# Optimization experiments

Hardware: AMD Instinct MI355X
Metric: run time of the kernel (lower is better)

The kernel has to match this reference:

```python
import jax, jax.numpy as jnp
import numpy as np

SELF_OBS_DIM = 18
NBR_OBS_DIM = 6
K = 6          # num_use_neighbor_obs
H = 128        # neighbor_hidden_size
B = 65536


def _mlp2(x, w1, b1, w2, b2):
    # two fc layers each followed by tanh nonlinearity
    x = jnp.tanh(x @ w1 + b1)
    return jnp.tanh(x @ w2 + b2)


def setup_inputs() -> dict:
    key = jax.random.key(0)
    ks = jax.random.split(key, 12)

    def w(k, i, o):
        return jax.random.normal(k, (i, o), dtype=jnp.float32) * (1.0 / np.sqrt(i))

    return {
        "self_obs": jax.random.normal(ks[0], (B, SELF_OBS_DIM), dtype=jnp.float32),
        "obs": jax.random.normal(ks[1], (B, SELF_OBS_DIM + K * NBR_OBS_DIM), dtype=jnp.float32),
        # embedding_mlp: (self_obs_dim + nbr_obs_dim) -> H -> H
        "e_w1": w(ks[2], SELF_OBS_DIM + NBR_OBS_DIM, H), "e_b1": jnp.zeros((H,), jnp.float32),
        "e_w2": w(ks[3], H, H), "e_b2": jnp.zeros((H,), jnp.float32),
        # neighbor_value_mlp: H -> H -> H
        "v_w1": w(ks[4], H, H), "v_b1": jnp.zeros((H,), jnp.float32),
        "v_w2": w(ks[5], H, H), "v_b2": jnp.zeros((H,), jnp.float32),
        # attention_mlp: 2H -> H -> H -> 1
        "a_w1": w(ks[6], 2 * H, H), "a_b1": jnp.zeros((H,), jnp.float32),
        "a_w2": w(ks[7], H, H), "a_b2": jnp.zeros((H,), jnp.float32),
        "a_w3": w(ks[8], H, 1), "a_b3": jnp.zeros((1,), jnp.float32),
        "all_neighbor_obs_size": K * NBR_OBS_DIM,
        "batch_size": B,
    }


def reference(self_obs, obs, e_w1, e_b1, e_w2, e_b2, v_w1, v_b1, v_w2, v_b2,
              a_w1, a_b1, a_w2, a_b2, a_w3, a_b3, all_neighbor_obs_size, batch_size):
    # slice neighbor obs and flatten: row i -> (batch i//K, neighbor i%K)
    obs_neighbors = obs[:, SELF_OBS_DIM:SELF_OBS_DIM + all_neighbor_obs_size]
    obs_neighbors = obs_neighbors.reshape(-1, NBR_OBS_DIM)            # [B*K, 6]
    # torch .repeat(K, 1): tile whole batch K times -> row i -> batch i % B
    self_obs_repeat = jnp.tile(self_obs, (K, 1))                       # [B*K, 18]
    mlp_input = jnp.concatenate((self_obs_repeat, obs_neighbors), axis=1)

    neighbor_embeddings = _mlp2(mlp_input, e_w1, e_b1, e_w2, e_b2)     # [B*K, H]
    neighbor_values = _mlp2(neighbor_embeddings, v_w1, v_b1, v_w2, v_b2)

    emb_mean = jnp.mean(neighbor_embeddings.reshape(batch_size, -1, H), axis=1)  # [B, H]
    emb_mean_repeat = jnp.tile(emb_mean, (K, 1))                       # [B*K, H]

    att_in = jnp.concatenate((neighbor_embeddings, emb_mean_repeat), axis=1)     # [B*K, 2H]
    att_h = jnp.tanh(att_in @ a_w1 + a_b1)
    att_h = jnp.tanh(att_h @ a_w2 + a_b2)
    att_logits = (att_h @ a_w3 + a_b3).reshape(batch_size, -1)         # [B, K]

    att = jax.nn.softmax(att_logits, axis=1).reshape(-1, 1)            # [B*K, 1]
    weighted = (att * neighbor_values).reshape(batch_size, -1, H)      # [B, K, H]
    return jnp.sum(weighted, axis=1)                                   # [B, H]
```

## Files before the change

kernel.cpp:

```cpp
#include <hip/hip_runtime.h>

typedef _Float16 f16;
typedef f16   f16x8 __attribute__((ext_vector_type(8)));
typedef float f32x4 __attribute__((ext_vector_type(4)));
typedef unsigned int uint;

#define NB     65536
#define NROWS  (NB*6)
#define NTILES 4096
#define TPB    16

#define OFF_E1 0
#define OFF_E2 4096
#define OFF_V1 20480
#define OFF_V2 36864
#define OFF_A1 53248
#define OFF_A2 86016
#define WFRAG_TOTAL 102400

#define EMB_BYTE_OFF   204800ull
#define MEANH_BYTE_OFF (204800ull + 100663296ull)

#define LDS_FENCE() asm volatile("s_waitcnt lgkmcnt(0)" ::: "memory")
#define WAIT_VM0()  asm volatile("s_waitcnt vmcnt(0)" ::: "memory")
#define BAR()       { __builtin_amdgcn_s_barrier(); __builtin_amdgcn_sched_barrier(0); }

__device__ __forceinline__ float tanh_fast(float x) {
  float e = __expf(2.0f * x);
  return 1.0f - 2.0f * __builtin_amdgcn_rcpf(e + 1.0f);
}

__global__ void prep_weights(const float* __restrict__ e1, const float* __restrict__ e2,
                             const float* __restrict__ v1, const float* __restrict__ v2,
                             const float* __restrict__ a1, const float* __restrict__ a2,
                             f16* __restrict__ dst)
{
  int i = blockIdx.x * 256 + threadIdx.x;
  if (i >= WFRAG_TOTAL) return;
  const float* src; int base, Ksrc;
  if      (i < OFF_E2) { src = e1; base = OFF_E1; Ksrc = 24;  }
  else if (i < OFF_V1) { src = e2; base = OFF_E2; Ksrc = 128; }
  else if (i < OFF_V2) { src = v1; base = OFF_V1; Ksrc = 128; }
  else if (i < OFF_A1) { src = v2; base = OFF_V2; Ksrc = 128; }
  else if (i < OFF_A2) { src = a1; base = OFF_A1; Ksrc = 256; }
  else                 { src = a2; base = OFF_A2; Ksrc = 128; }
  int li   = i - base;
  int j    = li & 7;
  int lane = (li >> 3) & 63;
  int nt   = (li >> 9) & 7;
  int kc   = li >> 12;
  int k = kc*32 + (lane >> 4)*8 + j;
  int n = nt*16 + (lane & 15);
  float v = (k < Ksrc) ? src[k*128 + n] : 0.0f;
  dst[i] = (f16)v;
}

__device__ __forceinline__ void mfma2(f32x4* acc, f16x8 a0, f16x8 a1, const f16* Wb, int lane)
{
  #pragma unroll
  for (int nt = 0; nt < 8; ++nt) {
    f16x8 w = *(const f16x8*)(Wb + (nt*64 + lane)*8);
    acc[nt] = __builtin_amdgcn_mfma_f32_16x16x32_f16(a0, w, acc[nt], 0, 0, 0);
  }
  #pragma unroll
  for (int nt = 0; nt < 8; ++nt) {
    f16x8 w = *(const f16x8*)(Wb + ((8+nt)*64 + lane)*8);
    acc[nt] = __builtin_amdgcn_mfma_f32_16x16x32_f16(a1, w, acc[nt], 0, 0, 0);
  }
}

__device__ __forceinline__ void epi_tanh_store(char* tb, const f32x4* acc, const float* bias8,
                                               int wid, int lane)
{
  int col0 = lane & 15, q = lane >> 4;
  #pragma unroll
  for (int nt = 0; nt < 8; ++nt) {
    #pragma unroll
    for (int rg = 0; rg < 4; ++rg) {
      int row = wid*16 + q*4 + rg;
      float h = tanh_fast(acc[nt][rg] + bias8[nt]);
      int byte = (row*256 + (nt*16 + col0)*2) ^ ((row & 7) << 4);
      *(f16*)(tb + byte) = (f16)h;
    }
  }
}

__device__ __forceinline__ void read_h_frags(const char* tb, f16x8* frag, int wid, int lane)
{
  int c = lane >> 4, rr = lane & 15;
  int row = wid*16 + rr;
  #pragma unroll
  for (int kc = 0; kc < 4; ++kc) {
    int byte = (row*256 + kc*64 + c*16) ^ ((row & 7) << 4);
    frag[kc] = *(const f16x8*)(tb + byte);
  }
}

__device__ __forceinline__ void gload_lds16(const f16* g, f16* l) {
  __builtin_amdgcn_global_load_lds(
    (const __attribute__((address_space(1))) unsigned int*)g,
    (__attribute__((address_space(3))) unsigned int*)l, 16, 0, 0);
}

__device__ __forceinline__ f16x8 gather_x(const float* __restrict__ so, const float* __restrict__ obs,
                                          int r, int c)
{
  int rs = r & (NB - 1);
  uint rq = (uint)r / 6u;
  uint rm = (uint)r - rq*6u;
  float xv[8] = {0.f,0.f,0.f,0.f,0.f,0.f,0.f,0.f};
  if (c == 0) {
    #pragma unroll
    for (int j = 0; j < 8; ++j) xv[j] = so[rs*18 + j];
  } else if (c == 1) {
    #pragma unroll
    for (int j = 0; j < 8; ++j) xv[j] = so[rs*18 + 8 + j];
  } else if (c == 2) {
    xv[0] = so[rs*18 + 16];
    xv[1] = so[rs*18 + 17];
    const float* nb = obs + (size_t)rq*54 + 18 + rm*6;
    #pragma unroll
    for (int j = 0; j < 6; ++j) xv[2+j] = nb[j];
  }
  f16x8 f;
  #pragma unroll
  for (int j = 0; j < 8; ++j) f[j] = (f16)xv[j];
  return f;
}

__global__ void __launch_bounds__(384, 1) enc_kernel(
  const float* __restrict__ self_obs, const float* __restrict__ obs,
  const float* __restrict__ e_b1, const float* __restrict__ e_b2,
  const float* __restrict__ a_b1,
  const f16* __restrict__ wfrag, f16* __restrict__ emb_out, f16* __restrict__ meanh_out)
{
  __shared__ __align__(16) f16 wE1[4096];
  __shared__ __align__(16) f16 wE2[16384];
  __shared__ __align__(16) f16 wA1m[16384];
  __shared__ __align__(16) char tbuf[24576];
  __shared__ __align__(16) char mbuf[4096];

  int tid = threadIdx.x, lane = tid & 63, wid = tid >> 6;
  int c = lane >> 4, rr = lane & 15;

  #pragma unroll
  for (int it = 0; it < 2; ++it) { int idx = it*384 + tid; if (idx < 512)  gload_lds16(wfrag + OFF_E1 + idx*8, wE1 + idx*8); }
  #pragma unroll
  for (int it = 0; it < 6; ++it) { int idx = it*384 + tid; if (idx < 2048) gload_lds16(wfrag + OFF_E2 + idx*8, wE2 + idx*8); }
  #pragma unroll
  for (int it = 0; it < 6; ++it) { int idx = it*384 + tid; if (idx < 2048) gload_lds16(wfrag + OFF_A1 + 16384 + idx*8, wA1m + idx*8); }

  float b1r[8], b2r[8], ab1r[8];
  #pragma unroll
  for (int nt = 0; nt < 8; ++nt) {
    int col = nt*16 + rr;
    b1r[nt] = e_b1[col]; b2r[nt] = e_b2[col]; ab1r[nt] = a_b1[col];
  }

  int t0 = blockIdx.x * TPB;
  f16x8 xfrag = gather_x(self_obs, obs, t0*96 + wid*16 + rr, c);
  WAIT_VM0(); BAR();

  for (int i = 0; i < TPB; ++i) {
    int t = t0 + i;
    f32x4 acc[8];
    #pragma unroll
    for (int nt = 0; nt < 8; ++nt) acc[nt] = (f32x4){0.f,0.f,0.f,0.f};
    #pragma unroll
    for (int nt = 0; nt < 8; ++nt) {
      f16x8 w = *(const f16x8*)(wE1 + (nt*64 + lane)*8);
      acc[nt] = __builtin_amdgcn_mfma_f32_16x16x32_f16(xfrag, w, acc[nt], 0, 0, 0);
    }
    epi_tanh_store(tbuf, acc, b1r, wid, lane);
    LDS_FENCE();
    f16x8 hf[4];
    read_h_frags(tbuf, hf, wid, lane);

    f16x8 xnext = gather_x(self_obs, obs,
                           ((i+1 < TPB) ? (t+1) : t0)*96 + wid*16 + rr, c);

    f32x4 acc2[8];
    #pragma unroll
    for (int nt = 0; nt < 8; ++nt) acc2[nt] = (f32x4){0.f,0.f,0.f,0.f};
    mfma2(acc2, hf[0], hf[1], wE2,        lane);
    mfma2(acc2, hf[2], hf[3], wE2 + 8192, lane);
    epi_tanh_store(tbuf, acc2, b2r, wid, lane);
    LDS_FENCE(); BAR();

    size_t gbase = (size_t)t * (96*128);
    #pragma unroll
    for (int it2 = 0; it2 < 4; ++it2) {
      int idx = it2*384 + tid;
      int row = idx >> 4, ch = idx & 15;
      int byte = (row*256 + ch*16) ^ ((row & 7) << 4);
      *(uint4*)(emb_out + gbase + row*128 + ch*8) = *(const uint4*)(tbuf + byte);
    }
    for (int i2 = tid; i2 < 2048; i2 += 384) {
      int b = i2 >> 7, col = i2 & 127;
      float s = 0.f;
      #pragma unroll
      for (int k2 = 0; k2 < 6; ++k2) {
        int brow = b*6 + k2;
        int byte = (brow*256 + col*2) ^ ((brow & 7) << 4);
        s += (float)*(const f16*)(tbuf + byte);
      }
      int mb = (b*256 + col*2) ^ ((b & 7) << 4);
      *(f16*)(mbuf + mb) = (f16)(s * (1.0f/6.0f));
    }
    LDS_FENCE(); BAR();

    f16x8 mfr[4];
    read_h_frags(mbuf, mfr, 0, lane);
    LDS_FENCE(); BAR();
    f32x4 accm[8];
    #pragma unroll
    for (int nt = 0; nt < 8; ++nt) accm[nt] = (f32x4){0.f,0.f,0.f,0.f};
    mfma2(accm, mfr[0], mfr[1], wA1m,        lane);
    mfma2(accm, mfr[2], mfr[3], wA1m + 8192, lane);
    if (wid == 0) {
      #pragma unroll
      for (int nt = 0; nt < 8; ++nt) {
        #pragma unroll
        for (int rg = 0; rg < 4; ++rg) {
          int row = c*4 + rg;
          int byte = (row*256 + (nt*16 + rr)*2) ^ ((row & 7) << 4);
          *(f16*)(mbuf + byte) = (f16)(accm[nt][rg] + ab1r[nt]);
        }
      }
      LDS_FENCE();
      #pragma unroll
      for (int it2 = 0; it2 < 4; ++it2) {
        int slot = it2*64 + lane;
        int row = slot >> 4, ch = slot & 15;
        int byte = (row*256 + ch*16) ^ ((row & 7) << 4);
        *(uint4*)(meanh_out + (size_t)(t*16 + row)*128 + ch*8) = *(const uint4*)(mbuf + byte);
      }
      LDS_FENCE();
    }
    xfrag = xnext;
    BAR();
  }
}

__global__ void __launch_bounds__(384, 1) att_kernel(
  const f16* __restrict__ wfrag, const f16* __restrict__ emb, const f16* __restrict__ meanh,
  const float* __restrict__ a_b2, const float* __restrict__ a_w3, const float* __restrict__ a_b3,
  const float* __restrict__ v_b1, const float* __restrict__ v_b2,
  float* __restrict__ out)
{
  __shared__ __align__(16) f16 W[4][16384];
  __shared__ __align__(16) char tbuf[24576];
  __shared__ float partial[96][17];
  __shared__ float attv[96];

  int tid = threadIdx.x, lane = tid & 63, wid = tid >> 6;
  int c = lane >> 4, rr = lane & 15;

  #pragma unroll
  for (int m = 0; m < 4; ++m) {
    const int offs[4] = {OFF_A1, OFF_A2, OFF_V1, OFF_V2};
    const f16* s = wfrag + offs[m];
    #pragma unroll
    for (int it = 0; it < 6; ++it) {
      int idx = it*384 + tid;
      if (idx < 2048) gload_lds16(s + idx*8, &W[m][0] + idx*8);
    }
  }

  float aw3r[8], ab2r[8], vb1r[8], vb2r[8];
  #pragma unroll
  for (int nt = 0; nt < 8; ++nt) {
    int col = nt*16 + rr;
    aw3r[nt] = a_w3[col]; ab2r[nt] = a_b2[col]; vb1r[nt] = v_b1[col]; vb2r[nt] = v_b2[col];
  }
  float ab3r = a_b3[0];

  int t0 = blockIdx.x * TPB;
  f16x8 ef[4];
  {
    size_t r = (size_t)t0*96 + wid*16 + rr;
    #pragma unroll
    for (int kc = 0; kc < 4; ++kc) ef[kc] = *(const f16x8*)(emb + r*128 + kc*32 + c*8);
  }
  WAIT_VM0(); BAR();

  for (int i = 0; i < TPB; ++i) {
    int t = t0 + i;
    int rowbase = t*96;

    #pragma unroll
    for (int it = 0; it < 4; ++it) {
      int slot = (wid*4 + it)*64 + lane;
      int row = slot >> 4, ch = slot & 15;
      int gr = (rowbase + row) & (NB - 1);
      gload_lds16(meanh + (size_t)gr*128 + (ch ^ (row & 7))*8, (f16*)(tbuf + slot*16));
    }

    f32x4 acc[8];
    #pragma unroll
    for (int nt = 0; nt < 8; ++nt) acc[nt] = (f32x4){0.f,0.f,0.f,0.f};
    mfma2(acc, ef[0], ef[1], &W[0][0],    lane);
    mfma2(acc, ef[2], ef[3], &W[0][8192], lane);
    WAIT_VM0(); BAR();

    f16x8 efn[4];
    {
      int tn = (i+1 < TPB) ? (t+1) : t;
      size_t r = (size_t)tn*96 + wid*16 + rr;
      #pragma unroll
      for (int kc = 0; kc < 4; ++kc) efn[kc] = *(const f16x8*)(emb + r*128 + kc*32 + c*8);
    }

    #pragma unroll
    for (int nt = 0; nt < 8; ++nt) {
      #pragma unroll
      for (int rg = 0; rg < 4; ++rg) {
        int row = wid*16 + c*4 + rg;
        int byte = (row*256 + (nt*16 + rr)*2) ^ ((row & 7) << 4);
        float mh = (float)*(const f16*)(tbuf + byte);
        float h = tanh_fast(acc[nt][rg] + mh);
        *(f16*)(tbuf + byte) = (f16)h;
      }
    }
    LDS_FENCE();
    f16x8 hf[4];
    read_h_frags(tbuf, hf, wid, lane);

    f32x4 acc2[8];
    #pragma unroll
    for (int nt = 0; nt < 8; ++nt) acc2[nt] = (f32x4){0.f,0.f,0.f,0.f};
    mfma2(acc2, hf[0], hf[1], &W[1][0],    lane);
    mfma2(acc2, hf[2], hf[3], &W[1][8192], lane);

    float part[4] = {0.f,0.f,0.f,0.f};
    #pragma unroll
    for (int nt = 0; nt < 8; ++nt) {
      float w3 = aw3r[nt], bb = ab2r[nt];
      #pragma unroll
      for (int rg = 0; rg < 4; ++rg) part[rg] += tanh_fast(acc2[nt][rg] + bb) * w3;
    }
    #pragma unroll
    for (int rg = 0; rg < 4; ++rg) partial[wid*16 + c*4 + rg][rr] = part[rg];
    LDS_FENCE(); BAR();
    if (tid < 96) {
      float s = ab3r;
      #pragma unroll
      for (int cc = 0; cc < 16; ++cc) s += partial[tid][cc];
      attv[tid] = s;
    }
    LDS_FENCE(); BAR();
    if (tid < 16) {
      float l[6]; float m = -1e30f;
      #pragma unroll
      for (int k2 = 0; k2 < 6; ++k2) { l[k2] = attv[tid*6 + k2]; m = fmaxf(m, l[k2]); }
      float ss = 0.f;
      #pragma unroll
      for (int k2 = 0; k2 < 6; ++k2) { l[k2] = __expf(l[k2] - m); ss += l[k2]; }
      float inv = __builtin_amdgcn_rcpf(ss);
      #pragma unroll
      for (int k2 = 0; k2 < 6; ++k2) attv[tid*6 + k2] = l[k2] * inv;
    }
    LDS_FENCE(); BAR();

    f32x4 acc3[8];
    #pragma unroll
    for (int nt = 0; nt < 8; ++nt) acc3[nt] = (f32x4){0.f,0.f,0.f,0.f};
    mfma2(acc3, ef[0], ef[1], &W[2][0],    lane);
    mfma2(acc3, ef[2], ef[3], &W[2][8192], lane);
    epi_tanh_store(tbuf, acc3, vb1r, wid, lane);
    LDS_FENCE();
    read_h_frags(tbuf, hf, wid, lane);

    f32x4 acc4[8];
    #pragma unroll
    for (int nt = 0; nt < 8; ++nt) acc4[nt] = (f32x4){0.f,0.f,0.f,0.f};
    mfma2(acc4, hf[0], hf[1], &W[3][0],    lane);
    mfma2(acc4, hf[2], hf[3], &W[3][8192], lane);

    #pragma unroll
    for (int nt = 0; nt < 8; ++nt) {
      float bb = vb2r[nt];
      #pragma unroll
      for (int rg = 0; rg < 4; ++rg) {
        int brow = wid*16 + c*4 + rg;
        float v = tanh_fast(acc4[nt][rg] + bb) * attv[brow];
        int byte = (brow*256 + (nt*16 + rr)*2) ^ ((brow & 7) << 4);
        *(f16*)(tbuf + byte) = (f16)v;
      }
    }
    LDS_FENCE(); BAR();

    int b0 = t*16;
    for (int i2 = tid; i2 < 2048; i2 += 384) {
      int b = i2 >> 7, col = i2 & 127;
      float s = 0.f;
      #pragma unroll
      for (int k2 = 0; k2 < 6; ++k2) {
        int brow = b*6 + k2;
        int byte = (brow*256 + col*2) ^ ((brow & 7) << 4);
        s += (float)*(const f16*)(tbuf + byte);
      }
      out[(size_t)(b0 + b)*128 + col] = s;
    }
    LDS_FENCE(); BAR();

    #pragma unroll
    for (int kc = 0; kc < 4; ++kc) ef[kc] = efn[kc];
  }
}

extern "C" void kernel_launch(void* const* d_in, const int* in_sizes, int n_in,
                              void* d_out, int out_size, void* d_ws, size_t ws_size,
                              hipStream_t stream)
{
  const float* self_obs = (const float*)d_in[0];
  const float* obs  = (const float*)d_in[1];
  const float* e_w1 = (const float*)d_in[2];
  const float* e_b1 = (const float*)d_in[3];
  const float* e_w2 = (const float*)d_in[4];
  const float* e_b2 = (const float*)d_in[5];
  const float* v_w1 = (const float*)d_in[6];
  const float* v_b1 = (const float*)d_in[7];
  const float* v_w2 = (const float*)d_in[8];
  const float* v_b2 = (const float*)d_in[9];
  const float* a_w1 = (const float*)d_in[10];
  const float* a_b1 = (const float*)d_in[11];
  const float* a_w2 = (const float*)d_in[12];
  const float* a_b2 = (const float*)d_in[13];
  const float* a_w3 = (const float*)d_in[14];
  const float* a_b3 = (const float*)d_in[15];

  f16*   wfrag = (f16*)d_ws;
  f16*   emb   = (f16*)((char*)d_ws + EMB_BYTE_OFF);
  f16*   meanh = (f16*)((char*)d_ws + MEANH_BYTE_OFF);
  float* out   = (float*)d_out;

  prep_weights<<<400, 256, 0, stream>>>(e_w1, e_w2, v_w1, v_w2, a_w1, a_w2, wfrag);
  enc_kernel<<<256, 384, 0, stream>>>(self_obs, obs, e_b1, e_b2, a_b1, wfrag, emb, meanh);
  att_kernel<<<256, 384, 0, stream>>>(wfrag, emb, meanh, a_b2, a_w3, a_b3, v_b1, v_b2, out);
}
```

Before: 365.3 us.

## Rebalance encoder grid, batch mean-projection MFMA, and use shuffle reduction in attention

The encoder kernel now runs 683 blocks of 6 tiles each instead of 256 blocks of 16, which spreads work over more CUs. It accumulates the 96 mean rows in a larger LDS buffer so the mean-to-attention projection runs once per block on all six waves, instead of once per tile on one wave. The attention kernel loads the projected means directly into registers in MFMA layout instead of staging them through LDS. It also replaces the partial-sum LDS reduction with warp shuffles and vectorizes the per-batch sum reductions and output stores. In exchange the encoder uses more LDS and more blocks, and the per-element mean gathers in the attention kernel are uncoalesced.

```diff
diff --git a/kernel.cpp b/kernel.cpp
--- a/kernel.cpp
+++ b/kernel.cpp
@@ -6,8 +6,6 @@
 typedef unsigned int uint;
 
 #define NB     65536
-#define NROWS  (NB*6)
-#define NTILES 4096
 #define TPB    16
 
 #define OFF_E1 0
@@ -19,11 +17,12 @@
 #define WFRAG_TOTAL 102400
 
 #define EMB_BYTE_OFF   204800ull
-#define MEANH_BYTE_OFF (204800ull + 100663296ull)
+#define PERM_BYTE_OFF  (204800ull + 100663296ull)
 
 #define LDS_FENCE() asm volatile("s_waitcnt lgkmcnt(0)" ::: "memory")
 #define WAIT_VM0()  asm volatile("s_waitcnt vmcnt(0)" ::: "memory")
 #define BAR()       { __builtin_amdgcn_s_barrier(); __builtin_amdgcn_sched_barrier(0); }
+#define SBAR()      __builtin_amdgcn_sched_barrier(0)
 
 __device__ __forceinline__ float tanh_fast(float x) {
   float e = __expf(2.0f * x);
@@ -101,6 +100,20 @@
     (const __attribute__((address_space(1))) unsigned int*)g,
     (__attribute__((address_space(3))) unsigned int*)l, 16, 0, 0);
 }
+__device__ __forceinline__ void stage32(const f16* g, f16* l, int tid) {
+  #pragma unroll
+  for (int it = 0; it < 6; ++it) {
+    int idx = (tid + it*384) & 2047;
+    gload_lds16(g + idx*8, l + idx*8);
+  }
+}
+__device__ __forceinline__ void stageE1(const f16* g, f16* l, int tid) {
+  #pragma unroll
+  for (int it = 0; it < 2; ++it) {
+    int idx = (tid + it*384) & 511;
+    gload_lds16(g + idx*8, l + idx*8);
+  }
+}
 
 __device__ __forceinline__ f16x8 gather_x(const float* __restrict__ so, const float* __restrict__ obs,
                                           int r, int c)
@@ -132,183 +145,173 @@
   const float* __restrict__ self_obs, const float* __restrict__ obs,
   const float* __restrict__ e_b1, const float* __restrict__ e_b2,
   const float* __restrict__ a_b1,
-  const f16* __restrict__ wfrag, f16* __restrict__ emb_out, f16* __restrict__ meanh_out)
-{
-  __shared__ __align__(16) f16 wE1[4096];
-  __shared__ __align__(16) f16 wE2[16384];
-  __shared__ __align__(16) f16 wA1m[16384];
+  const f16* __restrict__ wfrag, f16* __restrict__ emb_out, f16* __restrict__ perm_out)
+{
+  __shared__ __align__(16) f16 E1b[4096];
+  __shared__ __align__(16) f16 E2b[16384];
+  __shared__ __align__(16) f16 A1m[16384];
   __shared__ __align__(16) char tbuf[24576];
-  __shared__ __align__(16) char mbuf[4096];
+  __shared__ __align__(16) char mbuf[24576];
 
   int tid = threadIdx.x, lane = tid & 63, wid = tid >> 6;
   int c = lane >> 4, rr = lane & 15;
 
-  #pragma unroll
-  for (int it = 0; it < 2; ++it) { int idx = it*384 + tid; if (idx < 512)  gload_lds16(wfrag + OFF_E1 + idx*8, wE1 + idx*8); }
-  #pragma unroll
-  for (int it = 0; it < 6; ++it) { int idx = it*384 + tid; if (idx < 2048) gload_lds16(wfrag + OFF_E2 + idx*8, wE2 + idx*8); }
-  #pragma unroll
-  for (int it = 0; it < 6; ++it) { int idx = it*384 + tid; if (idx < 2048) gload_lds16(wfrag + OFF_A1 + 16384 + idx*8, wA1m + idx*8); }
-
-  float b1r[8], b2r[8], ab1r[8];
+  stageE1(wfrag + OFF_E1, E1b, tid);
+  stage32(wfrag + OFF_E2, E2b, tid);
+  stage32(wfrag + OFF_A1 + 16384, A1m, tid);
+
+  float eb1r[8], eb2r[8], ab1r[8];
   #pragma unroll
   for (int nt = 0; nt < 8; ++nt) {
     int col = nt*16 + rr;
-    b1r[nt] = e_b1[col]; b2r[nt] = e_b2[col]; ab1r[nt] = a_b1[col];
-  }
-
-  int t0 = blockIdx.x * TPB;
-  f16x8 xfrag = gather_x(self_obs, obs, t0*96 + wid*16 + rr, c);
+    eb1r[nt] = e_b1[col]; eb2r[nt] = e_b2[col]; ab1r[nt] = a_b1[col];
+  }
+
+  int S = blockIdx.x;
+  int T0 = S*6;
+  int jmax = 4096 - T0; if (jmax > 6) jmax = 6;
+
+  f16x8 xfrag = gather_x(self_obs, obs, T0*96 + wid*16 + rr, c);
   WAIT_VM0(); BAR();
 
-  for (int i = 0; i < TPB; ++i) {
-    int t = t0 + i;
-    f32x4 acc[8];
-    #pragma unroll
-    for (int nt = 0; nt < 8; ++nt) acc[nt] = (f32x4){0.f,0.f,0.f,0.f};
+  for (int j = 0; j < jmax; ++j) {
+    int T = T0 + j;
+    f32x4 acc1[8];
+    #pragma unroll
+    for (int nt = 0; nt < 8; ++nt) acc1[nt] = (f32x4){0.f,0.f,0.f,0.f};
     #pragma unroll
     for (int nt = 0; nt < 8; ++nt) {
-      f16x8 w = *(const f16x8*)(wE1 + (nt*64 + lane)*8);
-      acc[nt] = __builtin_amdgcn_mfma_f32_16x16x32_f16(xfrag, w, acc[nt], 0, 0, 0);
-    }
-    epi_tanh_store(tbuf, acc, b1r, wid, lane);
+      f16x8 w = *(const f16x8*)(E1b + (nt*64 + lane)*8);
+      acc1[nt] = __builtin_amdgcn_mfma_f32_16x16x32_f16(xfrag, w, acc1[nt], 0, 0, 0);
+    }
+    epi_tanh_store(tbuf, acc1, eb1r, wid, lane);
     LDS_FENCE();
     f16x8 hf[4];
     read_h_frags(tbuf, hf, wid, lane);
 
-    f16x8 xnext = gather_x(self_obs, obs,
-                           ((i+1 < TPB) ? (t+1) : t0)*96 + wid*16 + rr, c);
+    f16x8 xnext = xfrag;
+    if (j + 1 < jmax) xnext = gather_x(self_obs, obs, (T+1)*96 + wid*16 + rr, c);
 
     f32x4 acc2[8];
     #pragma unroll
     for (int nt = 0; nt < 8; ++nt) acc2[nt] = (f32x4){0.f,0.f,0.f,0.f};
-    mfma2(acc2, hf[0], hf[1], wE2,        lane);
-    mfma2(acc2, hf[2], hf[3], wE2 + 8192, lane);
-    epi_tanh_store(tbuf, acc2, b2r, wid, lane);
-    LDS_FENCE(); BAR();
-
-    size_t gbase = (size_t)t * (96*128);
-    #pragma unroll
-    for (int it2 = 0; it2 < 4; ++it2) {
-      int idx = it2*384 + tid;
-      int row = idx >> 4, ch = idx & 15;
-      int byte = (row*256 + ch*16) ^ ((row & 7) << 4);
-      *(uint4*)(emb_out + gbase + row*128 + ch*8) = *(const uint4*)(tbuf + byte);
-    }
-    for (int i2 = tid; i2 < 2048; i2 += 384) {
-      int b = i2 >> 7, col = i2 & 127;
-      float s = 0.f;
+    mfma2(acc2, hf[0], hf[1], E2b,        lane);
+    mfma2(acc2, hf[2], hf[3], E2b + 8192, lane);
+    epi_tanh_store(tbuf, acc2, eb2r, wid, lane);
+    LDS_FENCE();
+
+    {
+      size_t gbase = (size_t)T * (96*128);
+      #pragma unroll
+      for (int it = 0; it < 4; ++it) {
+        int idx = it*64 + lane;
+        int row = wid*16 + (idx >> 4), ch = idx & 15;
+        int byte = (row*256 + ch*16) ^ ((row & 7) << 4);
+        *(uint4*)(emb_out + gbase + (size_t)row*128 + ch*8) = *(const uint4*)(tbuf + byte);
+      }
+    }
+    BAR();
+    for (int i2 = tid; i2 < 1024; i2 += 384) {
+      int b = i2 >> 6, cp = i2 & 63;
+      float s0 = 0.f, s1 = 0.f;
       #pragma unroll
       for (int k2 = 0; k2 < 6; ++k2) {
         int brow = b*6 + k2;
-        int byte = (brow*256 + col*2) ^ ((brow & 7) << 4);
-        s += (float)*(const f16*)(tbuf + byte);
-      }
-      int mb = (b*256 + col*2) ^ ((b & 7) << 4);
-      *(f16*)(mbuf + mb) = (f16)(s * (1.0f/6.0f));
+        uint v = *(const uint*)(tbuf + ((brow*256 + cp*4) ^ ((brow & 7) << 4)));
+        s0 += (float)__builtin_bit_cast(f16, (unsigned short)(v & 0xffff));
+        s1 += (float)__builtin_bit_cast(f16, (unsigned short)(v >> 16));
+      }
+      f16 h0 = (f16)(s0 * (1.0f/6.0f)), h1 = (f16)(s1 * (1.0f/6.0f));
+      uint mv = (uint)__builtin_bit_cast(unsigned short, h0)
+              | ((uint)__builtin_bit_cast(unsigned short, h1) << 16);
+      int mrow = j*16 + b;
+      *(uint*)(mbuf + ((mrow*256 + cp*4) ^ ((mrow & 7) << 4))) = mv;
     }
     LDS_FENCE(); BAR();
-
-    f16x8 mfr[4];
-    read_h_frags(mbuf, mfr, 0, lane);
-    LDS_FENCE(); BAR();
-    f32x4 accm[8];
-    #pragma unroll
-    for (int nt = 0; nt < 8; ++nt) accm[nt] = (f32x4){0.f,0.f,0.f,0.f};
-    mfma2(accm, mfr[0], mfr[1], wA1m,        lane);
-    mfma2(accm, mfr[2], mfr[3], wA1m + 8192, lane);
-    if (wid == 0) {
-      #pragma unroll
-      for (int nt = 0; nt < 8; ++nt) {
-        #pragma unroll
-        for (int rg = 0; rg < 4; ++rg) {
-          int row = c*4 + rg;
-          int byte = (row*256 + (nt*16 + rr)*2) ^ ((row & 7) << 4);
-          *(f16*)(mbuf + byte) = (f16)(accm[nt][rg] + ab1r[nt]);
-        }
-      }
-      LDS_FENCE();
-      #pragma unroll
-      for (int it2 = 0; it2 < 4; ++it2) {
-        int slot = it2*64 + lane;
-        int row = slot >> 4, ch = slot & 15;
-        int byte = (row*256 + ch*16) ^ ((row & 7) << 4);
-        *(uint4*)(meanh_out + (size_t)(t*16 + row)*128 + ch*8) = *(const uint4*)(mbuf + byte);
-      }
-      LDS_FENCE();
-    }
     xfrag = xnext;
-    BAR();
+  }
+
+  f16x8 mfr[4];
+  read_h_frags(mbuf, mfr, wid, lane);
+  f32x4 accm[8];
+  #pragma unroll
+  for (int nt = 0; nt < 8; ++nt) accm[nt] = (f32x4){0.f,0.f,0.f,0.f};
+  mfma2(accm, mfr[0], mfr[1], A1m,        lane);
+  mfma2(accm, mfr[2], mfr[3], A1m + 8192, lane);
+
+  int gbase = S*96;
+  #pragma unroll
+  for (int rg = 0; rg < 4; ++rg) {
+    int m = gbase + wid*16 + c*4 + rg;
+    if (m < NB) {
+      f16x8 v;
+      #pragma unroll
+      for (int nt = 0; nt < 8; ++nt) v[nt] = (f16)(accm[nt][rg] + ab1r[nt]);
+      *(f16x8*)(perm_out + (size_t)m*128 + rr*8) = v;
+    }
   }
 }
 
 __global__ void __launch_bounds__(384, 1) att_kernel(
-  const f16* __restrict__ wfrag, const f16* __restrict__ emb, const f16* __restrict__ meanh,
+  const f16* __restrict__ wfrag, const f16* __restrict__ emb, const f16* __restrict__ perm,
   const float* __restrict__ a_b2, const float* __restrict__ a_w3, const float* __restrict__ a_b3,
   const float* __restrict__ v_b1, const float* __restrict__ v_b2,
   float* __restrict__ out)
 {
   __shared__ __align__(16) f16 W[4][16384];
   __shared__ __align__(16) char tbuf[24576];
-  __shared__ float partial[96][17];
   __shared__ float attv[96];
 
   int tid = threadIdx.x, lane = tid & 63, wid = tid >> 6;
   int c = lane >> 4, rr = lane & 15;
 
-  #pragma unroll
-  for (int m = 0; m < 4; ++m) {
-    const int offs[4] = {OFF_A1, OFF_A2, OFF_V1, OFF_V2};
-    const f16* s = wfrag + offs[m];
-    #pragma unroll
-    for (int it = 0; it < 6; ++it) {
-      int idx = it*384 + tid;
-      if (idx < 2048) gload_lds16(s + idx*8, &W[m][0] + idx*8);
-    }
-  }
-
-  float aw3r[8], ab2r[8], vb1r[8], vb2r[8];
+  stage32(wfrag + OFF_A1, &W[0][0], tid);
+  stage32(wfrag + OFF_A2, &W[1][0], tid);
+  stage32(wfrag + OFF_V1, &W[2][0], tid);
+  stage32(wfrag + OFF_V2, &W[3][0], tid);
+
+  float ab2r[8], aw3r[8], vb1r[8], vb2r[8];
   #pragma unroll
   for (int nt = 0; nt < 8; ++nt) {
     int col = nt*16 + rr;
-    aw3r[nt] = a_w3[col]; ab2r[nt] = a_b2[col]; vb1r[nt] = v_b1[col]; vb2r[nt] = v_b2[col];
+    ab2r[nt] = a_b2[col]; aw3r[nt] = a_w3[col]; vb1r[nt] = v_b1[col]; vb2r[nt] = v_b2[col];
   }
   float ab3r = a_b3[0];
 
   int t0 = blockIdx.x * TPB;
-  f16x8 ef[4];
+  f16x8 ef[4], mh[4];
   {
     size_t r = (size_t)t0*96 + wid*16 + rr;
     #pragma unroll
     for (int kc = 0; kc < 4; ++kc) ef[kc] = *(const f16x8*)(emb + r*128 + kc*32 + c*8);
+    #pragma unroll
+    for (int rg = 0; rg < 4; ++rg) {
+      int m = (t0*96 + wid*16 + c*4 + rg) & (NB - 1);
+      mh[rg] = *(const f16x8*)(perm + (size_t)m*128 + rr*8);
+    }
   }
   WAIT_VM0(); BAR();
 
   for (int i = 0; i < TPB; ++i) {
     int t = t0 + i;
-    int rowbase = t*96;
-
-    #pragma unroll
-    for (int it = 0; it < 4; ++it) {
-      int slot = (wid*4 + it)*64 + lane;
-      int row = slot >> 4, ch = slot & 15;
-      int gr = (rowbase + row) & (NB - 1);
-      gload_lds16(meanh + (size_t)gr*128 + (ch ^ (row & 7))*8, (f16*)(tbuf + slot*16));
-    }
-
-    f32x4 acc[8];
-    #pragma unroll
-    for (int nt = 0; nt < 8; ++nt) acc[nt] = (f32x4){0.f,0.f,0.f,0.f};
-    mfma2(acc, ef[0], ef[1], &W[0][0],    lane);
-    mfma2(acc, ef[2], ef[3], &W[0][8192], lane);
-    WAIT_VM0(); BAR();
-
-    f16x8 efn[4];
+
+    f32x4 acc3[8];
+    #pragma unroll
+    for (int nt = 0; nt < 8; ++nt) acc3[nt] = (f32x4){0.f,0.f,0.f,0.f};
+    mfma2(acc3, ef[0], ef[1], &W[0][0],    lane);
+    mfma2(acc3, ef[2], ef[3], &W[0][8192], lane);
+
+    f16x8 efn[4], mhn[4];
     {
       int tn = (i+1 < TPB) ? (t+1) : t;
       size_t r = (size_t)tn*96 + wid*16 + rr;
       #pragma unroll
       for (int kc = 0; kc < 4; ++kc) efn[kc] = *(const f16x8*)(emb + r*128 + kc*32 + c*8);
+      #pragma unroll
+      for (int rg = 0; rg < 4; ++rg) {
+        int m = (tn*96 + wid*16 + c*4 + rg) & (NB - 1);
+        mhn[rg] = *(const f16x8*)(perm + (size_t)m*128 + rr*8);
+      }
     }
 
     #pragma unroll
@@ -316,9 +319,8 @@
       #pragma unroll
       for (int rg = 0; rg < 4; ++rg) {
         int row = wid*16 + c*4 + rg;
+        float h = tanh_fast(acc3[nt][rg] + (float)mh[rg][nt]);
         int byte = (row*256 + (nt*16 + rr)*2) ^ ((row & 7) << 4);
-        float mh = (float)*(const f16*)(tbuf + byte);
-        float h = tanh_fast(acc[nt][rg] + mh);
         *(f16*)(tbuf + byte) = (f16)h;
       }
     }
@@ -326,27 +328,28 @@
     f16x8 hf[4];
     read_h_frags(tbuf, hf, wid, lane);
 
-    f32x4 acc2[8];
-    #pragma unroll
-    for (int nt = 0; nt < 8; ++nt) acc2[nt] = (f32x4){0.f,0.f,0.f,0.f};
-    mfma2(acc2, hf[0], hf[1], &W[1][0],    lane);
-    mfma2(acc2, hf[2], hf[3], &W[1][8192], lane);
+    f32x4 acc4[8];
+    #pragma unroll
+    for (int nt = 0; nt < 8; ++nt) acc4[nt] = (f32x4){0.f,0.f,0.f,0.f};
+    mfma2(acc4, hf[0], hf[1], &W[1][0],    lane);
+    mfma2(acc4, hf[2], hf[3], &W[1][8192], lane);
 
     float part[4] = {0.f,0.f,0.f,0.f};
     #pragma unroll
     for (int nt = 0; nt < 8; ++nt) {
-      float w3 = aw3r[nt], bb = ab2r[nt];
-      #pragma unroll
-      for (int rg = 0; rg < 4; ++rg) part[rg] += tanh_fast(acc2[nt][rg] + bb) * w3;
-    }
-    #pragma unroll
-    for (int rg = 0; rg < 4; ++rg) partial[wid*16 + c*4 + rg][rr] = part[rg];
-    LDS_FENCE(); BAR();
-    if (tid < 96) {
-      float s = ab3r;
-      #pragma unroll
-      for (int cc = 0; cc < 16; ++cc) s += partial[tid][cc];
-      attv[tid] = s;
+      #pragma unroll
+      for (int rg = 0; rg < 4; ++rg) part[rg] += tanh_fast(acc4[nt][rg] + ab2r[nt]) * aw3r[nt];
+    }
+    #pragma unroll
+    for (int rg = 0; rg < 4; ++rg) {
+      part[rg] += __shfl_xor(part[rg], 1);
+      part[rg] += __shfl_xor(part[rg], 2);
+      part[rg] += __shfl_xor(part[rg], 4);
+      part[rg] += __shfl_xor(part[rg], 8);
+    }
+    if (rr == 0) {
+      #pragma unroll
+      for (int rg = 0; rg < 4; ++rg) attv[wid*16 + c*4 + rg] = part[rg] + ab3r;
     }
     LDS_FENCE(); BAR();
     if (tid < 16) {
@@ -361,29 +364,31 @@
       for (int k2 = 0; k2 < 6; ++k2) attv[tid*6 + k2] = l[k2] * inv;
     }
     LDS_FENCE(); BAR();
-
-    f32x4 acc3[8];
-    #pragma unroll
-    for (int nt = 0; nt < 8; ++nt) acc3[nt] = (f32x4){0.f,0.f,0.f,0.f};
-    mfma2(acc3, ef[0], ef[1], &W[2][0],    lane);
-    mfma2(acc3, ef[2], ef[3], &W[2][8192], lane);
-    epi_tanh_store(tbuf, acc3, vb1r, wid, lane);
+    float attw[4];
+    #pragma unroll
+    for (int rg = 0; rg < 4; ++rg) attw[rg] = attv[wid*16 + c*4 + rg];
+
+    f32x4 acc5[8];
+    #pragma unroll
+    for (int nt = 0; nt < 8; ++nt) acc5[nt] = (f32x4){0.f,0.f,0.f,0.f};
+    mfma2(acc5, ef[0], ef[1], &W[2][0],    lane);
+    mfma2(acc5, ef[2], ef[3], &W[2][8192], lane);
+    epi_tanh_store(tbuf, acc5, vb1r, wid, lane);
     LDS_FENCE();
     read_h_frags(tbuf, hf, wid, lane);
 
-    f32x4 acc4[8];
-    #pragma unroll
-    for (int nt = 0; nt < 8; ++nt) acc4[nt] = (f32x4){0.f,0.f,0.f,0.f};
-    mfma2(acc4, hf[0], hf[1], &W[3][0],    lane);
-    mfma2(acc4, hf[2], hf[3], &W[3][8192], lane);
+    f32x4 acc6[8];
+    #pragma unroll
+    for (int nt = 0; nt < 8; ++nt) acc6[nt] = (f32x4){0.f,0.f,0.f,0.f};
+    mfma2(acc6, hf[0], hf[1], &W[3][0],    lane);
+    mfma2(acc6, hf[2], hf[3], &W[3][8192], lane);
 
     #pragma unroll
     for (int nt = 0; nt < 8; ++nt) {
-      float bb = vb2r[nt];
       #pragma unroll
       for (int rg = 0; rg < 4; ++rg) {
         int brow = wid*16 + c*4 + rg;
-        float v = tanh_fast(acc4[nt][rg] + bb) * attv[brow];
+        float v = tanh_fast(acc6[nt][rg] + vb2r[nt]) * attw[rg];
         int byte = (brow*256 + (nt*16 + rr)*2) ^ ((brow & 7) << 4);
         *(f16*)(tbuf + byte) = (f16)v;
       }
@@ -391,21 +396,25 @@
     LDS_FENCE(); BAR();
 
     int b0 = t*16;
-    for (int i2 = tid; i2 < 2048; i2 += 384) {
-      int b = i2 >> 7, col = i2 & 127;
-      float s = 0.f;
+    for (int i2 = tid; i2 < 1024; i2 += 384) {
+      int b = i2 >> 6, cp = i2 & 63;
+      float s0 = 0.f, s1 = 0.f;
       #pragma unroll
       for (int k2 = 0; k2 < 6; ++k2) {
         int brow = b*6 + k2;
-        int byte = (brow*256 + col*2) ^ ((brow & 7) << 4);
-        s += (float)*(const f16*)(tbuf + byte);
-      }
-      out[(size_t)(b0 + b)*128 + col] = s;
-    }
-    LDS_FENCE(); BAR();
+        uint v = *(const uint*)(tbuf + ((brow*256 + cp*4) ^ ((brow & 7) << 4)));
+        s0 += (float)__builtin_bit_cast(f16, (unsigned short)(v & 0xffff));
+        s1 += (float)__builtin_bit_cast(f16, (unsigned short)(v >> 16));
+      }
+      float2 st = {s0, s1};
+      *(float2*)(out + (size_t)(b0 + b)*128 + cp*2) = st;
+    }
+    BAR();
 
     #pragma unroll
     for (int kc = 0; kc < 4; ++kc) ef[kc] = efn[kc];
+    #pragma unroll
+    for (int rg = 0; rg < 4; ++rg) mh[rg] = mhn[rg];
   }
 }
 
@@ -432,10 +441,10 @@
 
   f16*   wfrag = (f16*)d_ws;
   f16*   emb   = (f16*)((char*)d_ws + EMB_BYTE_OFF);
-  f16*   meanh = (f16*)((char*)d_ws + MEANH_BYTE_OFF);
+  f16*   perm  = (f16*)((char*)d_ws + PERM_BYTE_OFF);
   float* out   = (float*)d_out;
 
   prep_weights<<<400, 256, 0, stream>>>(e_w1, e_w2, v_w1, v_w2, a_w1, a_w2, wfrag);
-  enc_kernel<<<256, 384, 0, stream>>>(self_obs, obs, e_b1, e_b2, a_b1, wfrag, emb, meanh);
-  att_kernel<<<256, 384, 0, stream>>>(wfrag, emb, meanh, a_b2, a_w3, a_b3, v_b1, v_b2, out);
-}
+  enc_kernel<<<683, 384, 0, stream>>>(self_obs, obs, e_b1, e_b2, a_b1, wfrag, emb, perm);
+  att_kernel<<<256, 384, 0, stream>>>(wfrag, emb, perm, a_b2, a_w3, a_b3, v_b1, v_b2, out);
+}
```

Measured after the change: 332.1 us. -9.1%, faster.
